# Kernel tuning notes

Measured on AMD Instinct MI355X. Metric: run time of the kernel, lower is better.

The kernel has to match this reference:

```python
import jax, jax.numpy as jnp
import numpy as np

N_NODES = 100000
N_EDGES = 1600000
IN_CH = 128
HID = 128
OUT_CH = 10
NUM_LAYERS = 3
NUM_GRAPHS = 512


def _glorot(key, shape):
    fan_in, fan_out = shape[0], shape[1]
    lim = jnp.sqrt(6.0 / (fan_in + fan_out))
    return jax.random.uniform(key, shape, jnp.float32, -lim, lim)


def setup_inputs() -> dict:
    key = jax.random.key(0)
    ks = jax.random.split(key, 20)
    inp = {}
    inp["x"] = jax.random.normal(ks[0], (N_NODES, IN_CH), jnp.float32)
    inp["edge_index"] = jax.random.randint(ks[1], (2, N_EDGES), 0, N_NODES, jnp.int64)
    inp["batch"] = jnp.sort(jax.random.randint(ks[2], (N_NODES,), 0, NUM_GRAPHS, jnp.int64))
    # GIN layer MLP params: Linear(in, hid) -> ReLU -> Linear(hid, hid)
    kidx = 3
    for l in range(NUM_LAYERS):
        d_in = IN_CH if l == 0 else HID
        inp[f"w1_{l}"] = _glorot(ks[kidx], (d_in, HID)); kidx += 1
        inp[f"b1_{l}"] = jnp.zeros((HID,), jnp.float32)
        inp[f"w2_{l}"] = _glorot(ks[kidx], (HID, HID)); kidx += 1
        inp[f"b2_{l}"] = jnp.zeros((HID,), jnp.float32)
    inp["lin_w"] = _glorot(ks[kidx], (HID, OUT_CH))
    inp["lin_b"] = jnp.zeros((OUT_CH,), jnp.float32)
    return inp


def _gin_forward(x, src, dst, batch, layer_params, lin_w, lin_b):
    h = x
    n_layers = len(layer_params)
    for i, (w1, b1, w2, b2) in enumerate(layer_params):
        # GINConv: (1 + eps) * h + sum_{j in N(i)} h_j, eps = 0
        agg = jax.ops.segment_sum(h[src], dst, num_segments=N_NODES)
        z = h + agg
        # MLP: Linear -> ReLU -> Linear
        h = jnp.maximum(z @ w1 + b1, 0.0) @ w2 + b2
        if i < n_layers - 1:  # inter-layer ReLU (PyG BasicGNN act)
            h = jnp.maximum(h, 0.0)
    # global_add_pool over batch ids -> [NUM_GRAPHS, HID]
    pooled = jax.ops.segment_sum(h, batch, num_segments=NUM_GRAPHS)
    # dropout(p=0.5) is identity in eval mode
    return pooled @ lin_w + lin_b


def reference(x, edge_index, batch,
              w1_0, b1_0, w2_0, b2_0,
              w1_1, b1_1, w2_1, b2_1,
              w1_2, b1_2, w2_2, b2_2,
              lin_w, lin_b):
    src, dst = edge_index[0], edge_index[1]
    layer_params = [(w1_0, b1_0, w2_0, b2_0),
                    (w1_1, b1_1, w2_1, b2_1),
                    (w1_2, b1_2, w2_2, b2_2)]
    return _gin_forward(x, src, dst, batch, layer_params, lin_w, lin_b)
```

## Files before the change

### kernel.cpp

```cpp
#include <hip/hip_runtime.h>

#define CH 128
#define OUTC 10
#define NB 256
#define BCAP 10240
#define PCHUNK 2048
#define PROWS 128

typedef __attribute__((ext_vector_type(8))) short short8;
typedef __attribute__((ext_vector_type(4))) float f32x4;


__device__ inline unsigned short f2bf(float f) {
    unsigned u = __builtin_bit_cast(unsigned, f);
    u += 0x7fffu + ((u >> 16) & 1u);
    return (unsigned short)(u >> 16);
}
__device__ inline float bf2f(unsigned short h) {
    unsigned u = ((unsigned)h) << 16;
    return __builtin_bit_cast(float, u);
}
__device__ inline float bflo(unsigned u) { return __builtin_bit_cast(float, u << 16); }
__device__ inline float bfhi(unsigned u) { return __builtin_bit_cast(float, u & 0xffff0000u); }


__global__ void convert_x_kernel(const float4* __restrict__ x4, uint2* __restrict__ xb, int n4) {
    int i = blockIdx.x * 256 + threadIdx.x;
    if (i < n4) {
        float4 v = x4[i];
        uint2 o;
        o.x = (unsigned)f2bf(v.x) | ((unsigned)f2bf(v.y) << 16);
        o.y = (unsigned)f2bf(v.z) | ((unsigned)f2bf(v.w) << 16);
        xb[i] = o;
    }
}


struct WPtrs { const float* s[6]; unsigned short* d[6]; };

__global__ void transpose_w_kernel(WPtrs p) {
    int m = blockIdx.y;
    int i = blockIdx.x * 256 + threadIdx.x;
    int k = i >> 7;
    int nn = i & 127;
    p.d[m][nn * CH + k] = f2bf(p.s[m][i]);
}


__global__ void partition_kernel(const int* __restrict__ src, const int* __restrict__ dst,
                                 int* __restrict__ bucketCnt, unsigned* __restrict__ pairs, int E) {
    __shared__ int hist[NB];
    __shared__ int base[NB];
    __shared__ int cur[NB];
    int tid = threadIdx.x;
    int e0 = blockIdx.x * PCHUNK;

    hist[tid] = 0;
    __syncthreads();
    #pragma unroll
    for (int i = 0; i < PCHUNK / 256; ++i) {
        int e = e0 + tid + i * 256;
        if (e < E) atomicAdd(&hist[dst[e] >> 9], 1);
    }
    __syncthreads();
    {
        int c = hist[tid];
        base[tid] = (c > 0) ? atomicAdd(&bucketCnt[tid], c) : 0;
        cur[tid] = 0;
    }
    __syncthreads();
    #pragma unroll
    for (int i = 0; i < PCHUNK / 256; ++i) {
        int e = e0 + tid + i * 256;
        if (e < E) {
            int d = dst[e];
            int bkt = d >> 9;
            int p = base[bkt] + atomicAdd(&cur[bkt], 1);
            if (p < BCAP)
                pairs[bkt * BCAP + p] = ((unsigned)(d & 511) << 17) | (unsigned)src[e];
        }
    }
}

__global__ void scan_buckets_kernel(const int* __restrict__ cnt, int* __restrict__ base) {
    __shared__ int sm[NB];
    int tid = threadIdx.x;
    sm[tid] = cnt[tid];
    __syncthreads();
    for (int off = 1; off < NB; off <<= 1) {
        int t = (tid >= off) ? sm[tid - off] : 0;
        __syncthreads();
        sm[tid] += t;
        __syncthreads();
    }
    base[tid] = sm[tid] - cnt[tid];
}


__launch_bounds__(256)
__global__ void build_csr_kernel(const unsigned* __restrict__ pairs, const int* __restrict__ bucketCnt,
                                 const int* __restrict__ bucketBase,
                                 int* __restrict__ offs, int* __restrict__ csr, int N) {
    __shared__ int ldeg[512];
    __shared__ int s0[512], s1[512];
    __shared__ int lexc[512];
    __shared__ int lcur[512];
    __shared__ int lcsr[BCAP];

    int b = blockIdx.x;
    int node0 = b << 9;
    if (node0 >= N) return;
    int nLocal = min(512, N - node0);
    int cnt = min(bucketCnt[b], BCAP);
    int gbase = bucketBase[b];
    int tid = threadIdx.x;

    for (int i = tid; i < 512; i += 256) ldeg[i] = 0;
    __syncthreads();
    for (int i = tid; i < cnt; i += 256)
        atomicAdd(&ldeg[pairs[b * BCAP + i] >> 17], 1);
    __syncthreads();

    for (int i = tid; i < 512; i += 256) s0[i] = ldeg[i];
    __syncthreads();
    int* sp = s0; int* dp = s1;
    for (int off = 1; off < 512; off <<= 1) {
        for (int i = tid; i < 512; i += 256)
            dp[i] = sp[i] + ((i >= off) ? sp[i - off] : 0);
        __syncthreads();
        int* t = sp; sp = dp; dp = t;
    }
    for (int i = tid; i < 512; i += 256) {
        int ex = sp[i] - ldeg[i];
        lexc[i] = ex;
        lcur[i] = ex;
    }
    __syncthreads();

    for (int i = tid; i < cnt; i += 256) {
        unsigned w = pairs[b * BCAP + i];
        int p = atomicAdd(&lcur[w >> 17], 1);
        lcsr[p] = (int)(w & 0x1ffffu);
    }
    __syncthreads();

    for (int i = tid; i < cnt; i += 256) csr[gbase + i] = lcsr[i];
    for (int i = tid; i < nLocal; i += 256) offs[node0 + i] = gbase + lexc[i];
    if (tid == 0 && node0 + nLocal == N) offs[N] = gbase + cnt;
}


__global__ void aggregate_kernel(const uint4* __restrict__ h4, const int* __restrict__ offs,
                                 const int* __restrict__ csr, uint4* __restrict__ z4, int n) {
    int node = blockIdx.x * 16 + (threadIdx.x >> 4);
    int lane = threadIdx.x & 15;
    if (node >= n) return;
    int beg = offs[node], end = offs[node + 1];

    float a[8];
    uint4 self = h4[node * 16 + lane];
    a[0] = bflo(self.x); a[1] = bfhi(self.x);
    a[2] = bflo(self.y); a[3] = bfhi(self.y);
    a[4] = bflo(self.z); a[5] = bfhi(self.z);
    a[6] = bflo(self.w); a[7] = bfhi(self.w);

    int e = beg;
    for (; e + 2 <= end; e += 2) {
        int s0 = csr[e], s1 = csr[e + 1];
        uint4 v0 = h4[s0 * 16 + lane];
        uint4 v1 = h4[s1 * 16 + lane];
        a[0] += bflo(v0.x); a[1] += bfhi(v0.x);
        a[2] += bflo(v0.y); a[3] += bfhi(v0.y);
        a[4] += bflo(v0.z); a[5] += bfhi(v0.z);
        a[6] += bflo(v0.w); a[7] += bfhi(v0.w);
        a[0] += bflo(v1.x); a[1] += bfhi(v1.x);
        a[2] += bflo(v1.y); a[3] += bfhi(v1.y);
        a[4] += bflo(v1.z); a[5] += bfhi(v1.z);
        a[6] += bflo(v1.w); a[7] += bfhi(v1.w);
    }
    if (e < end) {
        uint4 v = h4[csr[e] * 16 + lane];
        a[0] += bflo(v.x); a[1] += bfhi(v.x);
        a[2] += bflo(v.y); a[3] += bfhi(v.y);
        a[4] += bflo(v.z); a[5] += bfhi(v.z);
        a[6] += bflo(v.w); a[7] += bfhi(v.w);
    }
    uint4 o;
    o.x = (unsigned)f2bf(a[0]) | ((unsigned)f2bf(a[1]) << 16);
    o.y = (unsigned)f2bf(a[2]) | ((unsigned)f2bf(a[3]) << 16);
    o.z = (unsigned)f2bf(a[4]) | ((unsigned)f2bf(a[5]) << 16);
    o.w = (unsigned)f2bf(a[6]) | ((unsigned)f2bf(a[7]) << 16);
    z4[node * 16 + lane] = o;
}


#define PQ 136
#define BM 64

__launch_bounds__(256, 3)
__global__ void mlp_mfma_kernel(const unsigned short* __restrict__ z,
                                const unsigned short* __restrict__ w1t, const float* __restrict__ b1,
                                const unsigned short* __restrict__ w2t, const float* __restrict__ b2,
                                unsigned short* __restrict__ hout, int n, int relu_out) {
    __shared__ __align__(16) unsigned short zs[BM * PQ];
    __shared__ __align__(16) unsigned short ws[CH * PQ];

    int tid = threadIdx.x;
    int row0 = blockIdx.x * BM;
    int wv = tid >> 6;
    int lane = tid & 63;
    int lm = lane & 15;
    int lq = lane >> 4;

    for (int i = tid; i < BM * 16; i += 256) {
        int r = i >> 4, c = i & 15;
        int row = row0 + r;
        uint4 v = (row < n) ? ((const uint4*)z)[row * 16 + c] : make_uint4(0, 0, 0, 0);
        *(uint4*)((char*)zs + r * (PQ * 2) + c * 16) = v;
    }
    for (int i = tid; i < CH * 16; i += 256) {
        int r = i >> 4, c = i & 15;
        *(uint4*)((char*)ws + r * (PQ * 2) + c * 16) = ((const uint4*)w1t)[i];
    }
    __syncthreads();

    f32x4 acc[8];
    #pragma unroll
    for (int nt = 0; nt < 8; ++nt) {
        float bv = b1[nt * 16 + lm];
        acc[nt] = (f32x4){bv, bv, bv, bv};
    }
    int arow = wv * 16 + lm;
    #pragma unroll
    for (int kb = 0; kb < CH; kb += 32) {
        short8 afr = *(const short8*)&zs[arow * PQ + kb + 8 * lq];
        #pragma unroll
        for (int nt = 0; nt < 8; ++nt) {
            short8 bfr = *(const short8*)&ws[(nt * 16 + lm) * PQ + kb + 8 * lq];
            acc[nt] = __builtin_amdgcn_mfma_f32_16x16x32_bf16(afr, bfr, acc[nt], 0, 0, 0);
        }
    }
    __syncthreads();

    #pragma unroll
    for (int nt = 0; nt < 8; ++nt)
        #pragma unroll
        for (int r = 0; r < 4; ++r) {
            float v = fmaxf(acc[nt][r], 0.f);
            zs[(wv * 16 + lq * 4 + r) * PQ + nt * 16 + lm] = f2bf(v);
        }
    for (int i = tid; i < CH * 16; i += 256) {
        int r = i >> 4, c = i & 15;
        *(uint4*)((char*)ws + r * (PQ * 2) + c * 16) = ((const uint4*)w2t)[i];
    }
    __syncthreads();

    #pragma unroll
    for (int nt = 0; nt < 8; ++nt) {
        float bv = b2[nt * 16 + lm];
        acc[nt] = (f32x4){bv, bv, bv, bv};
    }
    #pragma unroll
    for (int kb = 0; kb < CH; kb += 32) {
        short8 afr = *(const short8*)&zs[arow * PQ + kb + 8 * lq];
        #pragma unroll
        for (int nt = 0; nt < 8; ++nt) {
            short8 bfr = *(const short8*)&ws[(nt * 16 + lm) * PQ + kb + 8 * lq];
            acc[nt] = __builtin_amdgcn_mfma_f32_16x16x32_bf16(afr, bfr, acc[nt], 0, 0, 0);
        }
    }
    __syncthreads();

    #pragma unroll
    for (int nt = 0; nt < 8; ++nt)
        #pragma unroll
        for (int r = 0; r < 4; ++r) {
            float v = acc[nt][r];
            if (relu_out) v = fmaxf(v, 0.f);
            zs[(wv * 16 + lq * 4 + r) * PQ + nt * 16 + lm] = f2bf(v);
        }
    __syncthreads();

    for (int i = tid; i < BM * 16; i += 256) {
        int r = i >> 4, c = i & 15;
        int row = row0 + r;
        if (row < n)
            ((uint4*)hout)[row * 16 + c] = *(const uint4*)((char*)zs + r * (PQ * 2) + c * 16);
    }
}


__global__ void pool_partial_kernel(const unsigned* __restrict__ h2, const int* __restrict__ batch,
                                    float* __restrict__ pooled, int n) {
    int r0 = blockIdx.x * PROWS;
    int tid = threadIdx.x;
    int c2 = tid & 63;
    int rs = tid >> 6;
    float a0 = 0.f, a1 = 0.f;
    int prevg = -1;
    #pragma unroll 4
    for (int i = 0; i < PROWS / 4; ++i) {
        int r = r0 + rs + i * 4;
        if (r >= n) break;
        int g = batch[r];
        if (g != prevg) {
            if (prevg >= 0) {
                atomicAdd(&pooled[prevg * CH + 2 * c2], a0);
                atomicAdd(&pooled[prevg * CH + 2 * c2 + 1], a1);
            }
            prevg = g; a0 = 0.f; a1 = 0.f;
        }
        unsigned v = h2[r * 64 + c2];
        a0 += bflo(v); a1 += bfhi(v);
    }
    if (prevg >= 0) {
        atomicAdd(&pooled[prevg * CH + 2 * c2], a0);
        atomicAdd(&pooled[prevg * CH + 2 * c2 + 1], a1);
    }
}

__global__ void final_linear_kernel(const float* __restrict__ pooled, const float* __restrict__ lin_w,
                                    const float* __restrict__ lin_b, float* __restrict__ out) {
    int g = blockIdx.x;
    int tid = threadIdx.x;
    __shared__ float pl[CH];
    pl[tid] = pooled[g * CH + tid];
    __syncthreads();
    if (tid < OUTC) {
        float a = lin_b[tid];
        #pragma unroll 16
        for (int c = 0; c < CH; ++c) a = fmaf(pl[c], lin_w[c * OUTC + tid], a);
        out[g * OUTC + tid] = a;
    }
}


static inline size_t aln(size_t x) { return (x + 255) & ~size_t(255); }

extern "C" void kernel_launch(void* const* d_in, const int* in_sizes, int n_in,
                              void* d_out, int out_size, void* d_ws, size_t ws_size,
                              hipStream_t stream) {
    const float* x      = (const float*)d_in[0];
    const int*   ei     = (const int*)d_in[1];
    const int*   batch  = (const int*)d_in[2];
    const float* w1[3]  = {(const float*)d_in[3], (const float*)d_in[7],  (const float*)d_in[11]};
    const float* b1[3]  = {(const float*)d_in[4], (const float*)d_in[8],  (const float*)d_in[12]};
    const float* w2[3]  = {(const float*)d_in[5], (const float*)d_in[9],  (const float*)d_in[13]};
    const float* b2[3]  = {(const float*)d_in[6], (const float*)d_in[10], (const float*)d_in[14]};
    const float* lin_w  = (const float*)d_in[15];
    const float* lin_b  = (const float*)d_in[16];
    float* out = (float*)d_out;

    int E = in_sizes[1] / 2;
    int N = in_sizes[2];
    int n_graphs = out_size / OUTC;
    const int* src = ei;
    const int* dst = ei + E;

    char* p = (char*)d_ws;
    int* bucketCnt  = (int*)p; p += aln(NB * 4);
    int* bucketBase = (int*)p; p += aln(NB * 4);
    unsigned* pairs = (unsigned*)p; p += aln((size_t)NB * BCAP * 4);
    int* offs       = (int*)p; p += aln((size_t)(N + 1) * 4);
    int* csr        = (int*)p; p += aln((size_t)E * 4);
    unsigned short* xb = (unsigned short*)p; p += aln((size_t)N * CH * 2);
    unsigned short* zb = (unsigned short*)p; p += aln((size_t)N * CH * 2);
    unsigned short* hb = (unsigned short*)p; p += aln((size_t)N * CH * 2);
    float* pooled = (float*)p; p += aln((size_t)n_graphs * CH * 4);
    unsigned short* wt[6];
    for (int i = 0; i < 6; ++i) { wt[i] = (unsigned short*)p; p += aln((size_t)CH * CH * 2); }
    (void)ws_size; (void)n_in;

    convert_x_kernel<<<(N * CH / 4 + 255) / 256, 256, 0, stream>>>((const float4*)x, (uint2*)xb, N * CH / 4);
    WPtrs wp;
    for (int l = 0; l < 3; ++l) {
        wp.s[2 * l] = w1[l];     wp.d[2 * l] = wt[2 * l];
        wp.s[2 * l + 1] = w2[l]; wp.d[2 * l + 1] = wt[2 * l + 1];
    }
    transpose_w_kernel<<<dim3(64, 6), 256, 0, stream>>>(wp);

    hipMemsetAsync(bucketCnt, 0, NB * 4, stream);
    partition_kernel<<<(E + PCHUNK - 1) / PCHUNK, 256, 0, stream>>>(src, dst, bucketCnt, pairs, E);
    scan_buckets_kernel<<<1, NB, 0, stream>>>(bucketCnt, bucketBase);
    build_csr_kernel<<<NB, 256, 0, stream>>>(pairs, bucketCnt, bucketBase, offs, csr, N);

    const unsigned short* hin = xb;
    for (int l = 0; l < 3; ++l) {
        aggregate_kernel<<<(N + 15) / 16, 256, 0, stream>>>(
            (const uint4*)hin, offs, csr, (uint4*)zb, N);
        mlp_mfma_kernel<<<(N + BM - 1) / BM, 256, 0, stream>>>(
            zb, wt[2 * l], b1[l], wt[2 * l + 1], b2[l], hb, N, (l < 2) ? 1 : 0);
        hin = hb;
    }

    hipMemsetAsync(pooled, 0, (size_t)n_graphs * CH * 4, stream);
    pool_partial_kernel<<<(N + PROWS - 1) / PROWS, 256, 0, stream>>>(
        (const unsigned*)hb, batch, pooled, N);
    final_linear_kernel<<<n_graphs, CH, 0, stream>>>(pooled, lin_w, lin_b, out);
}
```

Measured before the change: 464.8 us.

## Fuse neighbor aggregation, MLP and pooling into a single per-layer kernel

```diff
diff --git a/kernel.cpp b/kernel.cpp
--- a/kernel.cpp
+++ b/kernel.cpp
@@ -5,7 +5,6 @@
 #define NB 256
 #define BCAP 10240
 #define PCHUNK 2048
-#define PROWS 128
 
 typedef __attribute__((ext_vector_type(8))) short short8;
 typedef __attribute__((ext_vector_type(4))) float f32x4;
@@ -15,10 +14,6 @@
     unsigned u = __builtin_bit_cast(unsigned, f);
     u += 0x7fffu + ((u >> 16) & 1u);
     return (unsigned short)(u >> 16);
-}
-__device__ inline float bf2f(unsigned short h) {
-    unsigned u = ((unsigned)h) << 16;
-    return __builtin_bit_cast(float, u);
 }
 __device__ inline float bflo(unsigned u) { return __builtin_bit_cast(float, u << 16); }
 __device__ inline float bfhi(unsigned u) { return __builtin_bit_cast(float, u & 0xffff0000u); }
@@ -150,58 +145,17 @@
 }
 
 
-__global__ void aggregate_kernel(const uint4* __restrict__ h4, const int* __restrict__ offs,
-                                 const int* __restrict__ csr, uint4* __restrict__ z4, int n) {
-    int node = blockIdx.x * 16 + (threadIdx.x >> 4);
-    int lane = threadIdx.x & 15;
-    if (node >= n) return;
-    int beg = offs[node], end = offs[node + 1];
-
-    float a[8];
-    uint4 self = h4[node * 16 + lane];
-    a[0] = bflo(self.x); a[1] = bfhi(self.x);
-    a[2] = bflo(self.y); a[3] = bfhi(self.y);
-    a[4] = bflo(self.z); a[5] = bfhi(self.z);
-    a[6] = bflo(self.w); a[7] = bfhi(self.w);
-
-    int e = beg;
-    for (; e + 2 <= end; e += 2) {
-        int s0 = csr[e], s1 = csr[e + 1];
-        uint4 v0 = h4[s0 * 16 + lane];
-        uint4 v1 = h4[s1 * 16 + lane];
-        a[0] += bflo(v0.x); a[1] += bfhi(v0.x);
-        a[2] += bflo(v0.y); a[3] += bfhi(v0.y);
-        a[4] += bflo(v0.z); a[5] += bfhi(v0.z);
-        a[6] += bflo(v0.w); a[7] += bfhi(v0.w);
-        a[0] += bflo(v1.x); a[1] += bfhi(v1.x);
-        a[2] += bflo(v1.y); a[3] += bfhi(v1.y);
-        a[4] += bflo(v1.z); a[5] += bfhi(v1.z);
-        a[6] += bflo(v1.w); a[7] += bfhi(v1.w);
-    }
-    if (e < end) {
-        uint4 v = h4[csr[e] * 16 + lane];
-        a[0] += bflo(v.x); a[1] += bfhi(v.x);
-        a[2] += bflo(v.y); a[3] += bfhi(v.y);
-        a[4] += bflo(v.z); a[5] += bfhi(v.z);
-        a[6] += bflo(v.w); a[7] += bfhi(v.w);
-    }
-    uint4 o;
-    o.x = (unsigned)f2bf(a[0]) | ((unsigned)f2bf(a[1]) << 16);
-    o.y = (unsigned)f2bf(a[2]) | ((unsigned)f2bf(a[3]) << 16);
-    o.z = (unsigned)f2bf(a[4]) | ((unsigned)f2bf(a[5]) << 16);
-    o.w = (unsigned)f2bf(a[6]) | ((unsigned)f2bf(a[7]) << 16);
-    z4[node * 16 + lane] = o;
-}
-
-
 #define PQ 136
 #define BM 64
 
 __launch_bounds__(256, 3)
-__global__ void mlp_mfma_kernel(const unsigned short* __restrict__ z,
-                                const unsigned short* __restrict__ w1t, const float* __restrict__ b1,
-                                const unsigned short* __restrict__ w2t, const float* __restrict__ b2,
-                                unsigned short* __restrict__ hout, int n, int relu_out) {
+__global__ void gin_layer_kernel(const uint4* __restrict__ h4,
+                                 const int* __restrict__ offs, const int* __restrict__ csr,
+                                 const unsigned short* __restrict__ w1t, const float* __restrict__ b1,
+                                 const unsigned short* __restrict__ w2t, const float* __restrict__ b2,
+                                 unsigned short* __restrict__ hout,
+                                 const int* __restrict__ batch, float* __restrict__ pooled,
+                                 int n, int relu_out, int do_pool) {
     __shared__ __align__(16) unsigned short zs[BM * PQ];
     __shared__ __align__(16) unsigned short ws[CH * PQ];
 
@@ -212,15 +166,55 @@
     int lm = lane & 15;
     int lq = lane >> 4;
 
-    for (int i = tid; i < BM * 16; i += 256) {
-        int r = i >> 4, c = i & 15;
-        int row = row0 + r;
-        uint4 v = (row < n) ? ((const uint4*)z)[row * 16 + c] : make_uint4(0, 0, 0, 0);
-        *(uint4*)((char*)zs + r * (PQ * 2) + c * 16) = v;
-    }
     for (int i = tid; i < CH * 16; i += 256) {
         int r = i >> 4, c = i & 15;
         *(uint4*)((char*)ws + r * (PQ * 2) + c * 16) = ((const uint4*)w1t)[i];
+    }
+
+    {
+        int gl = tid & 15;
+        int grp = tid >> 4;
+        #pragma unroll
+        for (int it = 0; it < BM / 16; ++it) {
+            int rr = grp + 16 * it;
+            int node = row0 + rr;
+            uint4 o = make_uint4(0, 0, 0, 0);
+            if (node < n) {
+                int beg = offs[node], end = offs[node + 1];
+                float a[8];
+                uint4 self = h4[node * 16 + gl];
+                a[0] = bflo(self.x); a[1] = bfhi(self.x);
+                a[2] = bflo(self.y); a[3] = bfhi(self.y);
+                a[4] = bflo(self.z); a[5] = bfhi(self.z);
+                a[6] = bflo(self.w); a[7] = bfhi(self.w);
+                int e = beg;
+                for (; e + 2 <= end; e += 2) {
+                    int s0 = csr[e], s1 = csr[e + 1];
+                    uint4 v0 = h4[s0 * 16 + gl];
+                    uint4 v1 = h4[s1 * 16 + gl];
+                    a[0] += bflo(v0.x); a[1] += bfhi(v0.x);
+                    a[2] += bflo(v0.y); a[3] += bfhi(v0.y);
+                    a[4] += bflo(v0.z); a[5] += bfhi(v0.z);
+                    a[6] += bflo(v0.w); a[7] += bfhi(v0.w);
+                    a[0] += bflo(v1.x); a[1] += bfhi(v1.x);
+                    a[2] += bflo(v1.y); a[3] += bfhi(v1.y);
+                    a[4] += bflo(v1.z); a[5] += bfhi(v1.z);
+                    a[6] += bflo(v1.w); a[7] += bfhi(v1.w);
+                }
+                if (e < end) {
+                    uint4 v = h4[csr[e] * 16 + gl];
+                    a[0] += bflo(v.x); a[1] += bfhi(v.x);
+                    a[2] += bflo(v.y); a[3] += bfhi(v.y);
+                    a[4] += bflo(v.z); a[5] += bfhi(v.z);
+                    a[6] += bflo(v.w); a[7] += bfhi(v.w);
+                }
+                o.x = (unsigned)f2bf(a[0]) | ((unsigned)f2bf(a[1]) << 16);
+                o.y = (unsigned)f2bf(a[2]) | ((unsigned)f2bf(a[3]) << 16);
+                o.z = (unsigned)f2bf(a[4]) | ((unsigned)f2bf(a[5]) << 16);
+                o.w = (unsigned)f2bf(a[6]) | ((unsigned)f2bf(a[7]) << 16);
+            }
+            *(uint4*)((char*)zs + rr * (PQ * 2) + gl * 16) = o;
+        }
     }
     __syncthreads();
 
@@ -281,43 +275,41 @@
         }
     __syncthreads();
 
-    for (int i = tid; i < BM * 16; i += 256) {
-        int r = i >> 4, c = i & 15;
-        int row = row0 + r;
-        if (row < n)
-            ((uint4*)hout)[row * 16 + c] = *(const uint4*)((char*)zs + r * (PQ * 2) + c * 16);
-    }
-}
-
-
-__global__ void pool_partial_kernel(const unsigned* __restrict__ h2, const int* __restrict__ batch,
-                                    float* __restrict__ pooled, int n) {
-    int r0 = blockIdx.x * PROWS;
-    int tid = threadIdx.x;
-    int c2 = tid & 63;
-    int rs = tid >> 6;
-    float a0 = 0.f, a1 = 0.f;
-    int prevg = -1;
-    #pragma unroll 4
-    for (int i = 0; i < PROWS / 4; ++i) {
-        int r = r0 + rs + i * 4;
-        if (r >= n) break;
-        int g = batch[r];
-        if (g != prevg) {
-            if (prevg >= 0) {
-                atomicAdd(&pooled[prevg * CH + 2 * c2], a0);
-                atomicAdd(&pooled[prevg * CH + 2 * c2 + 1], a1);
+    if (!do_pool) {
+        for (int i = tid; i < BM * 16; i += 256) {
+            int r = i >> 4, c = i & 15;
+            int row = row0 + r;
+            if (row < n)
+                ((uint4*)hout)[row * 16 + c] = *(const uint4*)((char*)zs + r * (PQ * 2) + c * 16);
+        }
+    } else {
+        int c2 = tid & 63;
+        int rs = tid >> 6;
+        float a0 = 0.f, a1 = 0.f;
+        int prevg = -1;
+        #pragma unroll
+        for (int i = 0; i < BM / 4; ++i) {
+            int r = rs + 4 * i;
+            int row = row0 + r;
+            if (row >= n) break;
+            int g = batch[row];
+            if (g != prevg) {
+                if (prevg >= 0) {
+                    atomicAdd(&pooled[prevg * CH + 2 * c2], a0);
+                    atomicAdd(&pooled[prevg * CH + 2 * c2 + 1], a1);
+                }
+                prevg = g; a0 = 0.f; a1 = 0.f;
             }
-            prevg = g; a0 = 0.f; a1 = 0.f;
-        }
-        unsigned v = h2[r * 64 + c2];
-        a0 += bflo(v); a1 += bfhi(v);
-    }
-    if (prevg >= 0) {
-        atomicAdd(&pooled[prevg * CH + 2 * c2], a0);
-        atomicAdd(&pooled[prevg * CH + 2 * c2 + 1], a1);
-    }
-}
+            unsigned v = *(const unsigned*)((char*)zs + r * (PQ * 2) + c2 * 4);
+            a0 += bflo(v); a1 += bfhi(v);
+        }
+        if (prevg >= 0) {
+            atomicAdd(&pooled[prevg * CH + 2 * c2], a0);
+            atomicAdd(&pooled[prevg * CH + 2 * c2 + 1], a1);
+        }
+    }
+}
+
 
 __global__ void final_linear_kernel(const float* __restrict__ pooled, const float* __restrict__ lin_w,
                                     const float* __restrict__ lin_b, float* __restrict__ out) {
@@ -364,8 +356,8 @@
     int* offs       = (int*)p; p += aln((size_t)(N + 1) * 4);
     int* csr        = (int*)p; p += aln((size_t)E * 4);
     unsigned short* xb = (unsigned short*)p; p += aln((size_t)N * CH * 2);
-    unsigned short* zb = (unsigned short*)p; p += aln((size_t)N * CH * 2);
-    unsigned short* hb = (unsigned short*)p; p += aln((size_t)N * CH * 2);
+    unsigned short* hA = (unsigned short*)p; p += aln((size_t)N * CH * 2);
+    unsigned short* hB = (unsigned short*)p; p += aln((size_t)N * CH * 2);
     float* pooled = (float*)p; p += aln((size_t)n_graphs * CH * 4);
     unsigned short* wt[6];
     for (int i = 0; i < 6; ++i) { wt[i] = (unsigned short*)p; p += aln((size_t)CH * CH * 2); }
@@ -384,17 +376,15 @@
     scan_buckets_kernel<<<1, NB, 0, stream>>>(bucketCnt, bucketBase);
     build_csr_kernel<<<NB, 256, 0, stream>>>(pairs, bucketCnt, bucketBase, offs, csr, N);
 
-    const unsigned short* hin = xb;
-    for (int l = 0; l < 3; ++l) {
-        aggregate_kernel<<<(N + 15) / 16, 256, 0, stream>>>(
-            (const uint4*)hin, offs, csr, (uint4*)zb, N);
-        mlp_mfma_kernel<<<(N + BM - 1) / BM, 256, 0, stream>>>(
-            zb, wt[2 * l], b1[l], wt[2 * l + 1], b2[l], hb, N, (l < 2) ? 1 : 0);
-        hin = hb;
-    }
-
     hipMemsetAsync(pooled, 0, (size_t)n_graphs * CH * 4, stream);
-    pool_partial_kernel<<<(N + PROWS - 1) / PROWS, 256, 0, stream>>>(
-        (const unsigned*)hb, batch, pooled, N);
+
+    int nblk = (N + BM - 1) / BM;
+    gin_layer_kernel<<<nblk, 256, 0, stream>>>((const uint4*)xb, offs, csr,
+        wt[0], b1[0], wt[1], b2[0], hA, batch, pooled, N, 1, 0);
+    gin_layer_kernel<<<nblk, 256, 0, stream>>>((const uint4*)hA, offs, csr,
+        wt[2], b1[1], wt[3], b2[1], hB, batch, pooled, N, 1, 0);
+    gin_layer_kernel<<<nblk, 256, 0, stream>>>((const uint4*)hB, offs, csr,
+        wt[4], b1[2], wt[5], b2[2], hA, batch, pooled, N, 0, 1);
+
     final_linear_kernel<<<n_graphs, CH, 0, stream>>>(pooled, lin_w, lin_b, out);
 }
```

Measured after the change: 549.2 us. 18.2% more time.
